# Kernel optimization log

Measured on AMD Instinct MI355X. Metric: run time of the kernel, lower is better.

Reference implementation:

```python
import jax, jax.numpy as jnp
import numpy as np
import math

HIDDEN = 768
KEY = 128      # attention_key_size
INTER = 1536   # intermediate_size
B, S = 4, 2048


def setup_inputs() -> dict:
    key = jax.random.key(0)
    ks = jax.random.split(key, 8)
    hidden_states = jax.random.normal(ks[0], (B, S, HIDDEN), dtype=jnp.float32)
    attention_mask = jax.random.randint(ks[1], (B, 1, 1, S), 0, 2, dtype=jnp.int32)
    position_ids = jnp.arange(B * S, dtype=jnp.int32).reshape(B, S) % S
    Wi = jax.random.normal(ks[2], (HIDDEN, 2 * INTER + KEY), dtype=jnp.float32) * 0.02
    bi = jnp.zeros((2 * INTER + KEY,), dtype=jnp.float32)
    gamma = jax.random.normal(ks[3], (2, KEY), dtype=jnp.float32) * 0.02 + 1.0
    beta = jnp.zeros((2, KEY), dtype=jnp.float32)
    Wo = jax.random.normal(ks[4], (INTER, HIDDEN), dtype=jnp.float32) * 0.02
    bo = jnp.zeros((HIDDEN,), dtype=jnp.float32)
    return {"hidden_states": hidden_states, "attention_mask": attention_mask,
            "position_ids": position_ids, "Wi": Wi, "bi": bi,
            "gamma": gamma, "beta": beta, "Wo": Wo, "bo": bo}


def _gau_forward(hidden_states, attention_mask, Wi, bi, gamma, beta, Wo, bo):
    # i_dense + swish activation
    h = jax.nn.silu(jnp.einsum('bsd,de->bse', hidden_states, Wi) + bi)
    u = h[..., :INTER]
    v = h[..., INTER:2 * INTER]
    qk = h[..., 2 * INTER:]
    # OffsetScale: per-head affine (heads=2 -> q, k)
    q = qk * gamma[0] + beta[0]
    k = qk * gamma[1] + beta[1]
    scores = jnp.einsum('bid,bjd->bij', q, k) / math.sqrt(KEY)
    # additive mask: (1 - m) * -1e12, squeeze head dim
    am = (1.0 - attention_mask.astype(scores.dtype)) * -1e12
    scores = scores + am[:, 0]  # [B,1,S] broadcasts over query dim
    # softmax_plus normalization: scale logits by log(l)/log(512)
    valid = (scores > -1e11).astype(scores.dtype)
    l = jnp.maximum(jnp.sum(valid, axis=-1, keepdims=True), 1.0)
    scale = jnp.log(l) / jnp.log(jnp.asarray(512.0, scores.dtype))
    attn = jax.nn.softmax(scores * scale, axis=-1)
    ctx = jnp.einsum('bij,bjd->bid', attn, v)
    return jnp.einsum('bse,eh->bsh', u * ctx, Wo) + bo


def reference(hidden_states, attention_mask, position_ids, Wi, bi, gamma, beta, Wo, bo):
    # position_ids unused: p_bias is not 'rotary'
    return _gau_forward(hidden_states, attention_mask, Wi, bi, gamma, beta, Wo, bo)
```

## Files before the change

kernel.cpp:

```cpp
#include <hip/hip_runtime.h>
#include <math.h>

#define HIDDEN 768
#define KEY    128
#define INTER  1536
#define NB     4
#define SEQ    2048
#define MTOT   (NB*SEQ)
#define ETOT   (2*INTER+KEY)
#define CS     136

typedef short bf16x8 __attribute__((ext_vector_type(8)));
typedef float f32x4  __attribute__((ext_vector_type(4)));
typedef unsigned short u16x8 __attribute__((ext_vector_type(8)));

__device__ __forceinline__ unsigned short f2bfbits(float x) {
    union { float f; unsigned int u; } a; a.f = x;
    unsigned int r = a.u + 0x7fffu + ((a.u >> 16) & 1u);
    return (unsigned short)(r >> 16);
}
__device__ __forceinline__ float bfbits2f(unsigned short b) {
    union { float f; unsigned int u; } a; a.u = ((unsigned int)b) << 16;
    return a.f;
}

__device__ __forceinline__ void gl2lds16(const unsigned short* g, unsigned short* l) {
    __builtin_amdgcn_global_load_lds(
        (const __attribute__((address_space(1))) unsigned int*)g,
        (__attribute__((address_space(3))) unsigned int*)l, 16, 0, 0);
}

__global__ __launch_bounds__(256) void scale_kernel(const int* __restrict__ mask,
                                                    float* __restrict__ scaleb) {
    __shared__ int red[256];
    int b = blockIdx.x;
    int s = 0;
    for (int j = threadIdx.x; j < SEQ; j += 256)
        s += (mask[b*SEQ + j] != 0) ? 1 : 0;
    red[threadIdx.x] = s;
    __syncthreads();
    for (int step = 128; step > 0; step >>= 1) {
        if (threadIdx.x < step) red[threadIdx.x] += red[threadIdx.x + step];
        __syncthreads();
    }
    if (threadIdx.x == 0) {
        float l = fmaxf((float)red[0], 1.0f);
        scaleb[b] = logf(l) / logf(512.0f);
    }
}

__global__ __launch_bounds__(256) void cvt_bf16_kernel(const float* __restrict__ in,
                                                       unsigned short* __restrict__ out, int n4) {
    int i = blockIdx.x*256 + threadIdx.x;
    if (i < n4) {
        float4 v = ((const float4*)in)[i];
        ushort4 o;
        o.x = f2bfbits(v.x); o.y = f2bfbits(v.y);
        o.z = f2bfbits(v.z); o.w = f2bfbits(v.w);
        ((ushort4*)out)[i] = o;
    }
}

__global__ __launch_bounds__(256) void transpose_cvt(const float* __restrict__ in,
                                                     unsigned short* __restrict__ out,
                                                     int R, int C) {
    __shared__ unsigned short tile[32][33];
    int c0 = blockIdx.x*32, r0 = blockIdx.y*32;
    int tx = threadIdx.x & 31, ty4 = (threadIdx.x >> 5)*4;
    #pragma unroll
    for (int rr = 0; rr < 4; rr++) {
        int r = ty4 + rr;
        tile[r][tx] = f2bfbits(in[(size_t)(r0+r)*C + c0+tx]);
    }
    __syncthreads();
    #pragma unroll
    for (int rr = 0; rr < 4; rr++) {
        int r = ty4 + rr;
        out[(size_t)(c0+r)*R + r0+tx] = tile[tx][r];
    }
}

template<int BK>
__device__ __forceinline__ void mfma_core(
    const unsigned short* __restrict__ Abase, int lda,
    const unsigned short* __restrict__ Bbase, int ldb,
    unsigned short* As, unsigned short* Bs,
    f32x4 acc[4][4], int tid, int ktot)
{
    const int lane = tid & 63, wave = tid >> 6;
    const int wm = (wave >> 1) << 6, wn = (wave & 1) << 6;
    const int lm = lane & 15;
    const int q8 = (lane >> 4) << 3;
    const int row_a = tid >> 2, col_a = (tid & 3) << 3;
    const int row_b = row_a + 64;

    for (int k0 = 0; k0 < ktot; k0 += BK) {
        if (k0) __syncthreads();
        #pragma unroll
        for (int h = 0; h < BK/32; h++) {
            gl2lds16(Abase + (size_t)row_a*lda + k0 + h*32 + col_a, As + h*4096 + tid*8);
            gl2lds16(Abase + (size_t)row_b*lda + k0 + h*32 + col_a, As + h*4096 + (tid+256)*8);
            gl2lds16(Bbase + (size_t)row_a*ldb + k0 + h*32 + col_a, Bs + h*4096 + tid*8);
            gl2lds16(Bbase + (size_t)row_b*ldb + k0 + h*32 + col_a, Bs + h*4096 + (tid+256)*8);
        }
        __syncthreads();
        #pragma unroll
        for (int h = 0; h < BK/32; h++) {
            const unsigned short* Ah = As + h*4096;
            const unsigned short* Bh = Bs + h*4096;
            bf16x8 af[4], bfr[4];
            #pragma unroll
            for (int i = 0; i < 4; i++)
                af[i] = *(const bf16x8*)&Ah[(wm + i*16 + lm)*32 + q8];
            #pragma unroll
            for (int j = 0; j < 4; j++)
                bfr[j] = *(const bf16x8*)&Bh[(wn + j*16 + lm)*32 + q8];
            #pragma unroll
            for (int i = 0; i < 4; i++)
                #pragma unroll
                for (int j = 0; j < 4; j++)
                    acc[i][j] = __builtin_amdgcn_mfma_f32_16x16x32_bf16(af[i], bfr[j], acc[i][j], 0, 0, 0);
        }
    }
}

#define EPILOG_IDX \
    const int lane = tid & 63, wave = tid >> 6; \
    const int wm = (wave >> 1) << 6, wn = (wave & 1) << 6; \
    const int cn = lane & 15, r4 = (lane >> 4) << 2;

__global__ __launch_bounds__(256) void gemm1_mfma(
    const unsigned short* __restrict__ Xb, const unsigned short* __restrict__ WiT,
    const float* __restrict__ bi, const float* __restrict__ gamma, const float* __restrict__ beta,
    unsigned short* __restrict__ u, unsigned short* __restrict__ vT,
    unsigned short* __restrict__ qb, unsigned short* __restrict__ kb)
{
    __shared__ __align__(16) unsigned short smem[128*CS];
    unsigned short* As = smem;
    unsigned short* Bs = smem + 4096;
    const int tid = threadIdx.x;
    const int bid = blockIdx.x;
    const int xcd = bid & 7, slot = bid >> 3;
    const int xt = slot >> 3;
    const int yt = (xcd << 3) + (slot & 7);
    const int row0 = yt*128, col0 = xt*128;
    f32x4 acc[4][4];
    #pragma unroll
    for (int i = 0; i < 4; i++)
        #pragma unroll
        for (int j = 0; j < 4; j++)
            acc[i][j] = (f32x4){0.f,0.f,0.f,0.f};
    mfma_core<32>(Xb + (size_t)row0*HIDDEN, HIDDEN, WiT + (size_t)col0*HIDDEN, HIDDEN,
                  As, Bs, acc, tid, HIDDEN);
    EPILOG_IDX
    __syncthreads();
    #pragma unroll
    for (int j = 0; j < 4; j++) {
        int nl = wn + j*16 + cn;
        float bin = bi[col0 + nl];
        #pragma unroll
        for (int i = 0; i < 4; i++) {
            #pragma unroll
            for (int r = 0; r < 4; r++) {
                int rowl = wm + i*16 + r4 + r;
                float x = acc[i][j][r] + bin;
                float h = x / (1.0f + __expf(-x));
                smem[rowl*CS + nl] = f2bfbits(h);
            }
        }
    }
    __syncthreads();
    if (col0 < INTER) {
        #pragma unroll
        for (int rnd = 0; rnd < 8; rnd++) {
            int row = rnd*16 + (tid>>4);
            int col = (tid&15)*8;
            u16x8 h = *(const u16x8*)&smem[row*CS + col];
            *(u16x8*)&u[(size_t)(row0+row)*INTER + col0 + col] = h;
        }
    } else if (col0 < 2*INTER) {
        int c = tid >> 1;
        int half = tid & 1;
        int b = row0 / SEQ;
        int srow = row0 - b*SEQ + half*64;
        size_t base = ((size_t)b*INTER + (col0 - INTER) + c)*SEQ + srow;
        #pragma unroll
        for (int k = 0; k < 8; k++) {
            u16x8 h;
            #pragma unroll
            for (int t = 0; t < 8; t++)
                h[t] = smem[(half*64 + k*8 + t)*CS + c];
            *(u16x8*)&vT[base + k*8] = h;
        }
    } else {
        #pragma unroll
        for (int rnd = 0; rnd < 8; rnd++) {
            int row = rnd*16 + (tid>>4);
            int col = (tid&15)*8;
            u16x8 h = *(const u16x8*)&smem[row*CS + col];
            int m = row0 + row;
            u16x8 qo, ko;
            #pragma unroll
            for (int t = 0; t < 8; t++) {
                float hv = bfbits2f(h[t]);
                qo[t] = f2bfbits(hv*gamma[col+t]     + beta[col+t]);
                ko[t] = f2bfbits(hv*gamma[KEY+col+t] + beta[KEY+col+t]);
            }
            *(u16x8*)&qb[(size_t)m*KEY + col] = qo;
            *(u16x8*)&kb[(size_t)m*KEY + col] = ko;
        }
    }
}

__global__ __launch_bounds__(256) void attn_mfma(
    const unsigned short* __restrict__ qb, const unsigned short* __restrict__ kb,
    const int* __restrict__ mask, const float* __restrict__ scaleb,
    unsigned short* __restrict__ P)
{
    __shared__ __align__(16) unsigned short smem[128*CS];
    unsigned short* As = smem;
    unsigned short* Bs = smem + 8192;
    const int tid = threadIdx.x;
    const int z = blockIdx.z;
    const int row0 = blockIdx.y*128, col0 = blockIdx.x*128;
    f32x4 acc[4][4];
    #pragma unroll
    for (int i = 0; i < 4; i++)
        #pragma unroll
        for (int j = 0; j < 4; j++)
            acc[i][j] = (f32x4){0.f,0.f,0.f,0.f};
    mfma_core<64>(qb + ((size_t)z*SEQ + row0)*KEY, KEY, kb + ((size_t)z*SEQ + col0)*KEY, KEY,
                  As, Bs, acc, tid, KEY);
    const float st = scaleb[z] * 0.08838834764831845f;
    EPILOG_IDX
    __syncthreads();
    #pragma unroll
    for (int j = 0; j < 4; j++) {
        int nl = wn + j*16 + cn;
        float mkf = (mask[z*SEQ + col0 + nl] != 0) ? 1.0f : 0.0f;
        #pragma unroll
        for (int i = 0; i < 4; i++) {
            #pragma unroll
            for (int r = 0; r < 4; r++) {
                int rowl = wm + i*16 + r4 + r;
                float p = mkf * __expf(acc[i][j][r]*st);
                smem[rowl*CS + nl] = f2bfbits(p);
            }
        }
    }
    __syncthreads();
    #pragma unroll
    for (int rnd = 0; rnd < 8; rnd++) {
        int row = rnd*16 + (tid>>4);
        int col = (tid&15)*8;
        u16x8 h = *(const u16x8*)&smem[row*CS + col];
        *(u16x8*)&P[((size_t)z*SEQ + row0 + row)*SEQ + col0 + col] = h;
    }
}

__global__ __launch_bounds__(256) void rowsum_kernel(const unsigned short* __restrict__ P,
                                                     float* __restrict__ lbuf) {
    int row = blockIdx.x*4 + (threadIdx.x >> 6);
    int lane = threadIdx.x & 63;
    const unsigned short* pr = P + (size_t)row*SEQ;
    float s = 0.f;
    for (int c = lane*8; c < SEQ; c += 64*8) {
        ushort4 a = *(const ushort4*)&pr[c];
        ushort4 b = *(const ushort4*)&pr[c+4];
        s += bfbits2f(a.x)+bfbits2f(a.y)+bfbits2f(a.z)+bfbits2f(a.w)
           + bfbits2f(b.x)+bfbits2f(b.y)+bfbits2f(b.z)+bfbits2f(b.w);
    }
    #pragma unroll
    for (int off = 32; off > 0; off >>= 1) s += __shfl_down(s, off, 64);
    if (lane == 0) lbuf[row] = s;
}

__global__ __launch_bounds__(256) void pv_mfma(
    const unsigned short* __restrict__ P, const unsigned short* __restrict__ vT,
    const float* __restrict__ lbuf, unsigned short* __restrict__ u)
{
    __shared__ __align__(16) unsigned short smem[128*CS];
    unsigned short* As = smem;
    unsigned short* Bs = smem + 8192;
    const int tid = threadIdx.x;
    const int bid = blockIdx.x;
    const int xcd = bid & 7, slot = bid >> 3;
    const int z = slot / 24, pos = slot % 24;
    const int yt = (xcd & 3)*4 + pos/6;
    const int xt = (xcd >> 2)*6 + pos%6;
    const int row0 = yt*128, col0 = xt*128;
    f32x4 acc[4][4];
    #pragma unroll
    for (int i = 0; i < 4; i++)
        #pragma unroll
        for (int j = 0; j < 4; j++)
            acc[i][j] = (f32x4){0.f,0.f,0.f,0.f};
    mfma_core<64>(P + ((size_t)z*SEQ + row0)*SEQ, SEQ, vT + ((size_t)z*INTER + col0)*SEQ, SEQ,
                  As, Bs, acc, tid, SEQ);
    EPILOG_IDX
    __syncthreads();
    #pragma unroll
    for (int j = 0; j < 4; j++) {
        int nl = wn + j*16 + cn;
        #pragma unroll
        for (int i = 0; i < 4; i++) {
            #pragma unroll
            for (int r = 0; r < 4; r++) {
                int rowl = wm + i*16 + r4 + r;
                smem[rowl*CS + nl] = f2bfbits(acc[i][j][r]);
            }
        }
    }
    __syncthreads();
    #pragma unroll
    for (int rnd = 0; rnd < 8; rnd++) {
        int row = rnd*16 + (tid>>4);
        int col = (tid&15)*8;
        int m = z*SEQ + row0 + row;
        float linv = 1.0f / lbuf[m];
        u16x8 cx = *(const u16x8*)&smem[row*CS + col];
        size_t idx = (size_t)m*INTER + col0 + col;
        u16x8 uu = *(const u16x8*)&u[idx];
        u16x8 g;
        #pragma unroll
        for (int t = 0; t < 8; t++)
            g[t] = f2bfbits(bfbits2f(uu[t]) * bfbits2f(cx[t]) * linv);
        *(u16x8*)&u[idx] = g;
    }
}

__global__ __launch_bounds__(256) void gemm2_mfma(
    const unsigned short* __restrict__ g, const unsigned short* __restrict__ WoT,
    const float* __restrict__ bo, float* __restrict__ out)
{
    __shared__ __align__(16) unsigned short As[8192];
    __shared__ __align__(16) unsigned short Bs[8192];
    const int tid = threadIdx.x;
    const int bid = blockIdx.x;
    const int xcd = bid & 7, slot = bid >> 3;
    const int xt = slot >> 3;
    const int yt = (xcd << 3) + (slot & 7);
    const int row0 = yt*128, col0 = xt*128;
    f32x4 acc[4][4];
    #pragma unroll
    for (int i = 0; i < 4; i++)
        #pragma unroll
        for (int j = 0; j < 4; j++)
            acc[i][j] = (f32x4){0.f,0.f,0.f,0.f};
    mfma_core<64>(g + (size_t)row0*INTER, INTER, WoT + (size_t)col0*INTER, INTER,
                  As, Bs, acc, tid, INTER);
    EPILOG_IDX
    #pragma unroll
    for (int j = 0; j < 4; j++) {
        int n = col0 + wn + j*16 + cn;
        float bon = bo[n];
        #pragma unroll
        for (int i = 0; i < 4; i++) {
            #pragma unroll
            for (int r = 0; r < 4; r++) {
                int m = row0 + wm + i*16 + r4 + r;
                out[(size_t)m*HIDDEN + n] = acc[i][j][r] + bon;
            }
        }
    }
}

extern "C" void kernel_launch(void* const* d_in, const int* in_sizes, int n_in,
                              void* d_out, int out_size, void* d_ws, size_t ws_size,
                              hipStream_t stream)
{
    const float* X     = (const float*)d_in[0];
    const int*   mask  = (const int*)d_in[1];
    const float* Wi    = (const float*)d_in[3];
    const float* bi    = (const float*)d_in[4];
    const float* gamma = (const float*)d_in[5];
    const float* beta  = (const float*)d_in[6];
    const float* Wo    = (const float*)d_in[7];
    const float* bo    = (const float*)d_in[8];
    float* out = (float*)d_out;

    unsigned short* Xb  = (unsigned short*)d_ws;
    unsigned short* WiT = Xb  + (size_t)MTOT*HIDDEN;
    unsigned short* WoT = WiT + (size_t)ETOT*HIDDEN;
    unsigned short* u   = WoT + (size_t)HIDDEN*INTER;
    unsigned short* vT  = u   + (size_t)MTOT*INTER;
    unsigned short* qb  = vT  + (size_t)MTOT*INTER;
    unsigned short* kb  = qb  + (size_t)MTOT*KEY;
    unsigned short* P   = kb  + (size_t)MTOT*KEY;
    float* lb  = (float*)(P + (size_t)NB*SEQ*SEQ);
    float* scb = lb + MTOT;

    scale_kernel<<<NB, 256, 0, stream>>>(mask, scb);
    cvt_bf16_kernel<<<(MTOT*HIDDEN/4 + 255)/256, 256, 0, stream>>>(X, Xb, MTOT*HIDDEN/4);
    transpose_cvt<<<dim3(ETOT/32, HIDDEN/32), 256, 0, stream>>>(Wi, WiT, HIDDEN, ETOT);
    transpose_cvt<<<dim3(HIDDEN/32, INTER/32), 256, 0, stream>>>(Wo, WoT, INTER, HIDDEN);
    gemm1_mfma<<<1600, 256, 0, stream>>>(Xb, WiT, bi, gamma, beta, u, vT, qb, kb);
    attn_mfma<<<dim3(SEQ/128, SEQ/128, NB), 256, 0, stream>>>(qb, kb, mask, scb, P);
    rowsum_kernel<<<MTOT/4, 256, 0, stream>>>(P, lb);
    pv_mfma<<<768, 256, 0, stream>>>(P, vT, lb, u);
    gemm2_mfma<<<384, 256, 0, stream>>>(u, WoT, bo, out);
}
```

Before: 302.3 us.

## Fuse prep kernels, fold rowsum into attention epilogue, retile gemm2

Merges the bf16 conversion, the two weight transposes and the mask-scale reduction into a single prep launch. The separate rowsum pass over P is replaced by per-tile partial row sums written from the attention epilogue, which pv_mfma then adds up across 16 tiles. gemm2 moves to 128x64 tiles with 768 blocks to fill more CUs. The aim is fewer launches and no extra full read of P, at the cost of redundant partial-sum loads in each pv block and a hand-written gemm2 loop.

After: 289.3 us. 1.05x faster.

```diff
diff --git a/kernel.cpp b/kernel.cpp
--- a/kernel.cpp
+++ b/kernel.cpp
@@ -30,43 +30,11 @@
         (__attribute__((address_space(3))) unsigned int*)l, 16, 0, 0);
 }
 
-__global__ __launch_bounds__(256) void scale_kernel(const int* __restrict__ mask,
-                                                    float* __restrict__ scaleb) {
-    __shared__ int red[256];
-    int b = blockIdx.x;
-    int s = 0;
-    for (int j = threadIdx.x; j < SEQ; j += 256)
-        s += (mask[b*SEQ + j] != 0) ? 1 : 0;
-    red[threadIdx.x] = s;
-    __syncthreads();
-    for (int step = 128; step > 0; step >>= 1) {
-        if (threadIdx.x < step) red[threadIdx.x] += red[threadIdx.x + step];
-        __syncthreads();
-    }
-    if (threadIdx.x == 0) {
-        float l = fmaxf((float)red[0], 1.0f);
-        scaleb[b] = logf(l) / logf(512.0f);
-    }
-}
-
-__global__ __launch_bounds__(256) void cvt_bf16_kernel(const float* __restrict__ in,
-                                                       unsigned short* __restrict__ out, int n4) {
-    int i = blockIdx.x*256 + threadIdx.x;
-    if (i < n4) {
-        float4 v = ((const float4*)in)[i];
-        ushort4 o;
-        o.x = f2bfbits(v.x); o.y = f2bfbits(v.y);
-        o.z = f2bfbits(v.z); o.w = f2bfbits(v.w);
-        ((ushort4*)out)[i] = o;
-    }
-}
-
-__global__ __launch_bounds__(256) void transpose_cvt(const float* __restrict__ in,
-                                                     unsigned short* __restrict__ out,
-                                                     int R, int C) {
-    __shared__ unsigned short tile[32][33];
-    int c0 = blockIdx.x*32, r0 = blockIdx.y*32;
-    int tx = threadIdx.x & 31, ty4 = (threadIdx.x >> 5)*4;
+__device__ __forceinline__ void transpose_tile(
+    const float* __restrict__ in, unsigned short* __restrict__ out,
+    int R, int C, int c0, int r0, int tid, unsigned short tile[32][33])
+{
+    int tx = tid & 31, ty4 = (tid >> 5)*4;
     #pragma unroll
     for (int rr = 0; rr < 4; rr++) {
         int r = ty4 + rr;
@@ -77,6 +45,47 @@
     for (int rr = 0; rr < 4; rr++) {
         int r = ty4 + rr;
         out[(size_t)(c0+r)*R + r0+tx] = tile[tx][r];
+    }
+}
+
+__global__ __launch_bounds__(256) void prep_kernel(
+    const float* __restrict__ X, const float* __restrict__ Wi,
+    const float* __restrict__ Wo, const int* __restrict__ mask,
+    unsigned short* __restrict__ Xb, unsigned short* __restrict__ WiT,
+    unsigned short* __restrict__ WoT, float* __restrict__ scaleb)
+{
+    __shared__ unsigned short tile[32][33];
+    __shared__ int red[256];
+    const int bid = blockIdx.x, tid = threadIdx.x;
+    if (bid < 3072) {
+        int i = bid*256 + tid;
+        const float4* in4 = (const float4*)X;
+        float4 a = in4[(size_t)i*2], b = in4[(size_t)i*2+1];
+        u16x8 o;
+        o[0]=f2bfbits(a.x); o[1]=f2bfbits(a.y); o[2]=f2bfbits(a.z); o[3]=f2bfbits(a.w);
+        o[4]=f2bfbits(b.x); o[5]=f2bfbits(b.y); o[6]=f2bfbits(b.z); o[7]=f2bfbits(b.w);
+        *(u16x8*)&Xb[(size_t)i*8] = o;
+    } else if (bid < 5472) {
+        int t = bid - 3072;
+        transpose_tile(Wi, WiT, HIDDEN, ETOT, (t%100)*32, (t/100)*32, tid, tile);
+    } else if (bid < 6624) {
+        int t = bid - 5472;
+        transpose_tile(Wo, WoT, INTER, HIDDEN, (t%24)*32, (t/24)*32, tid, tile);
+    } else {
+        int b = bid - 6624;
+        int s = 0;
+        for (int j = tid; j < SEQ; j += 256)
+            s += (mask[b*SEQ + j] != 0) ? 1 : 0;
+        red[tid] = s;
+        __syncthreads();
+        for (int step = 128; step > 0; step >>= 1) {
+            if (tid < step) red[tid] += red[tid + step];
+            __syncthreads();
+        }
+        if (tid == 0) {
+            float l = fmaxf((float)red[0], 1.0f);
+            scaleb[b] = logf(l) / logf(512.0f);
+        }
     }
 }
 
@@ -215,7 +224,7 @@
 __global__ __launch_bounds__(256) void attn_mfma(
     const unsigned short* __restrict__ qb, const unsigned short* __restrict__ kb,
     const int* __restrict__ mask, const float* __restrict__ scaleb,
-    unsigned short* __restrict__ P)
+    unsigned short* __restrict__ P, float* __restrict__ lpart)
 {
     __shared__ __align__(16) unsigned short smem[128*CS];
     unsigned short* As = smem;
@@ -255,31 +264,22 @@
         int col = (tid&15)*8;
         u16x8 h = *(const u16x8*)&smem[row*CS + col];
         *(u16x8*)&P[((size_t)z*SEQ + row0 + row)*SEQ + col0 + col] = h;
-    }
-}
-
-__global__ __launch_bounds__(256) void rowsum_kernel(const unsigned short* __restrict__ P,
-                                                     float* __restrict__ lbuf) {
-    int row = blockIdx.x*4 + (threadIdx.x >> 6);
-    int lane = threadIdx.x & 63;
-    const unsigned short* pr = P + (size_t)row*SEQ;
-    float s = 0.f;
-    for (int c = lane*8; c < SEQ; c += 64*8) {
-        ushort4 a = *(const ushort4*)&pr[c];
-        ushort4 b = *(const ushort4*)&pr[c+4];
-        s += bfbits2f(a.x)+bfbits2f(a.y)+bfbits2f(a.z)+bfbits2f(a.w)
-           + bfbits2f(b.x)+bfbits2f(b.y)+bfbits2f(b.z)+bfbits2f(b.w);
-    }
-    #pragma unroll
-    for (int off = 32; off > 0; off >>= 1) s += __shfl_down(s, off, 64);
-    if (lane == 0) lbuf[row] = s;
+        float s8 = 0.f;
+        #pragma unroll
+        for (int t = 0; t < 8; t++) s8 += bfbits2f(h[t]);
+        #pragma unroll
+        for (int off = 8; off > 0; off >>= 1) s8 += __shfl_xor(s8, off, 16);
+        if ((tid & 15) == 0)
+            lpart[(size_t)blockIdx.x*MTOT + (size_t)z*SEQ + row0 + row] = s8;
+    }
 }
 
 __global__ __launch_bounds__(256) void pv_mfma(
     const unsigned short* __restrict__ P, const unsigned short* __restrict__ vT,
-    const float* __restrict__ lbuf, unsigned short* __restrict__ u)
+    const float* __restrict__ lpart, unsigned short* __restrict__ u)
 {
     __shared__ __align__(16) unsigned short smem[128*CS];
+    __shared__ float ls[128];
     unsigned short* As = smem;
     unsigned short* Bs = smem + 8192;
     const int tid = threadIdx.x;
@@ -289,6 +289,13 @@
     const int yt = (xcd & 3)*4 + pos/6;
     const int xt = (xcd >> 2)*6 + pos%6;
     const int row0 = yt*128, col0 = xt*128;
+    if (tid < 128) {
+        float s = 0.f;
+        #pragma unroll
+        for (int t = 0; t < 16; t++)
+            s += lpart[(size_t)t*MTOT + (size_t)z*SEQ + row0 + tid];
+        ls[tid] = s;
+    }
     f32x4 acc[4][4];
     #pragma unroll
     for (int i = 0; i < 4; i++)
@@ -317,7 +324,7 @@
         int row = rnd*16 + (tid>>4);
         int col = (tid&15)*8;
         int m = z*SEQ + row0 + row;
-        float linv = 1.0f / lbuf[m];
+        float linv = 1.0f / ls[row];
         u16x8 cx = *(const u16x8*)&smem[row*CS + col];
         size_t idx = (size_t)m*INTER + col0 + col;
         u16x8 uu = *(const u16x8*)&u[idx];
@@ -329,29 +336,62 @@
     }
 }
 
-__global__ __launch_bounds__(256) void gemm2_mfma(
+__global__ __launch_bounds__(256, 3) void gemm2_mfma(
     const unsigned short* __restrict__ g, const unsigned short* __restrict__ WoT,
     const float* __restrict__ bo, float* __restrict__ out)
 {
     __shared__ __align__(16) unsigned short As[8192];
-    __shared__ __align__(16) unsigned short Bs[8192];
+    __shared__ __align__(16) unsigned short Bs[4096];
     const int tid = threadIdx.x;
     const int bid = blockIdx.x;
     const int xcd = bid & 7, slot = bid >> 3;
     const int xt = slot >> 3;
     const int yt = (xcd << 3) + (slot & 7);
-    const int row0 = yt*128, col0 = xt*128;
-    f32x4 acc[4][4];
+    const int row0 = yt*128, col0 = xt*64;
+    const int lane = tid & 63, wave = tid >> 6;
+    const int wm = (wave >> 1) << 6;
+    const int wn = (wave & 1) << 5;
+    const int lm = lane & 15;
+    const int q8 = (lane >> 4) << 3;
+    const int row_a = tid >> 2, col_a = (tid & 3) << 3;
+    f32x4 acc[4][2];
     #pragma unroll
     for (int i = 0; i < 4; i++)
         #pragma unroll
-        for (int j = 0; j < 4; j++)
+        for (int j = 0; j < 2; j++)
             acc[i][j] = (f32x4){0.f,0.f,0.f,0.f};
-    mfma_core<64>(g + (size_t)row0*INTER, INTER, WoT + (size_t)col0*INTER, INTER,
-                  As, Bs, acc, tid, INTER);
-    EPILOG_IDX
-    #pragma unroll
-    for (int j = 0; j < 4; j++) {
+    const unsigned short* Abase = g + (size_t)row0*INTER;
+    const unsigned short* Bbase = WoT + (size_t)col0*INTER;
+    for (int k0 = 0; k0 < INTER; k0 += 64) {
+        if (k0) __syncthreads();
+        #pragma unroll
+        for (int h = 0; h < 2; h++) {
+            gl2lds16(Abase + (size_t)row_a*INTER + k0 + h*32 + col_a,      As + h*4096 + tid*8);
+            gl2lds16(Abase + (size_t)(row_a+64)*INTER + k0 + h*32 + col_a, As + h*4096 + (tid+256)*8);
+            gl2lds16(Bbase + (size_t)row_a*INTER + k0 + h*32 + col_a,      Bs + h*2048 + tid*8);
+        }
+        __syncthreads();
+        #pragma unroll
+        for (int h = 0; h < 2; h++) {
+            const unsigned short* Ah = As + h*4096;
+            const unsigned short* Bh = Bs + h*2048;
+            bf16x8 af[4], bfr[2];
+            #pragma unroll
+            for (int i = 0; i < 4; i++)
+                af[i] = *(const bf16x8*)&Ah[(wm + i*16 + lm)*32 + q8];
+            #pragma unroll
+            for (int j = 0; j < 2; j++)
+                bfr[j] = *(const bf16x8*)&Bh[(wn + j*16 + lm)*32 + q8];
+            #pragma unroll
+            for (int i = 0; i < 4; i++)
+                #pragma unroll
+                for (int j = 0; j < 2; j++)
+                    acc[i][j] = __builtin_amdgcn_mfma_f32_16x16x32_bf16(af[i], bfr[j], acc[i][j], 0, 0, 0);
+        }
+    }
+    const int cn = lane & 15, r4 = (lane >> 4) << 2;
+    #pragma unroll
+    for (int j = 0; j < 2; j++) {
         int n = col0 + wn + j*16 + cn;
         float bon = bo[n];
         #pragma unroll
@@ -387,16 +427,12 @@
     unsigned short* qb  = vT  + (size_t)MTOT*INTER;
     unsigned short* kb  = qb  + (size_t)MTOT*KEY;
     unsigned short* P   = kb  + (size_t)MTOT*KEY;
-    float* lb  = (float*)(P + (size_t)NB*SEQ*SEQ);
-    float* scb = lb + MTOT;
-
-    scale_kernel<<<NB, 256, 0, stream>>>(mask, scb);
-    cvt_bf16_kernel<<<(MTOT*HIDDEN/4 + 255)/256, 256, 0, stream>>>(X, Xb, MTOT*HIDDEN/4);
-    transpose_cvt<<<dim3(ETOT/32, HIDDEN/32), 256, 0, stream>>>(Wi, WiT, HIDDEN, ETOT);
-    transpose_cvt<<<dim3(HIDDEN/32, INTER/32), 256, 0, stream>>>(Wo, WoT, INTER, HIDDEN);
+    float* scb   = (float*)(P + (size_t)NB*SEQ*SEQ);
+    float* lpart = scb + 8;
+
+    prep_kernel<<<6628, 256, 0, stream>>>(X, Wi, Wo, mask, Xb, WiT, WoT, scb);
     gemm1_mfma<<<1600, 256, 0, stream>>>(Xb, WiT, bi, gamma, beta, u, vT, qb, kb);
-    attn_mfma<<<dim3(SEQ/128, SEQ/128, NB), 256, 0, stream>>>(qb, kb, mask, scb, P);
-    rowsum_kernel<<<MTOT/4, 256, 0, stream>>>(P, lb);
-    pv_mfma<<<768, 256, 0, stream>>>(P, vT, lb, u);
-    gemm2_mfma<<<384, 256, 0, stream>>>(u, WoT, bo, out);
-}
+    attn_mfma<<<dim3(SEQ/128, SEQ/128, NB), 256, 0, stream>>>(qb, kb, mask, scb, P, lpart);
+    pv_mfma<<<768, 256, 0, stream>>>(P, vT, lpart, u);
+    gemm2_mfma<<<768, 256, 0, stream>>>(u, WoT, bo, out);
+}
```
